# Performance work log

Measured on AMD Instinct MI355X. Metric: run time of the kernel, lower is better.

Reference implementation:

```python
import jax, jax.numpy as jnp
import numpy as np

N_NODES = 10000
T = 8
F_IN = 4
H1 = 16
HEADS = 4
H2 = 32
G = 32
PW = 16
E = 160000


def _gat(x, src, dst, W, a_src, a_dst, b, concat):
    # x: [T, N, Fin]; PyG GATConv (eval mode, dropout inactive), self-loops already in src/dst
    t, n, _ = x.shape
    heads, c = a_src.shape
    z = (x @ W).reshape(t, n, heads, c)                      # [T,N,H,C]
    asrc = jnp.einsum('tnhc,hc->tnh', z, a_src)
    adst = jnp.einsum('tnhc,hc->tnh', z, a_dst)
    e = jax.nn.leaky_relu(asrc[:, src] + adst[:, dst], 0.2)   # [T,E,H]
    e = e.transpose(1, 0, 2)                                  # [E,T,H]
    m = jax.ops.segment_max(e, dst, num_segments=n)           # [N,T,H]
    ex = jnp.exp(e - m[dst])
    s = jax.ops.segment_sum(ex, dst, num_segments=n)
    att = ex / s[dst]                                         # [E,T,H] softmax over in-edges of dst
    msg = z.transpose(1, 0, 2, 3)[src] * att[..., None]       # [E,T,H,C]
    out = jax.ops.segment_sum(msg, dst, num_segments=n)       # [N,T,H,C]
    out = out.transpose(1, 0, 2, 3)                           # [T,N,H,C]
    out = out.reshape(t, n, heads * c) if concat else out.mean(axis=2)
    return out + b


def _forward(dynamic, cI, cR, N, I, R, edge_index, h0,
             W1, att_src1, att_dst1, b1, W2, att_src2, att_dst2, b2,
             W_ih, W_hh, b_ih, b_hh, Wi, bi, Wr, br, Ws, bs):
    Npop = N.squeeze()
    loops = jnp.arange(N_NODES, dtype=edge_index.dtype)
    src = jnp.concatenate([edge_index[0], loops])
    dst = jnp.concatenate([edge_index[1], loops])
    x = dynamic.transpose(1, 0, 2)                            # [T,N,F] all timesteps batched
    x = jax.nn.elu(_gat(x, src, dst, W1, att_src1, att_dst1, b1, True))
    x = jax.nn.elu(_gat(x, src, dst, W2, att_src2, att_dst2, b2, False))
    cur_h = x.mean(axis=1)                                    # [T,H2]

    def gru_step(h, xt):  # torch GRUCell: gates in (r,z,n) order
        gi = W_ih @ xt + b_ih
        gh = W_hh @ h + b_hh
        ir, iz, inn = jnp.split(gi, 3)
        hr, hz, hn = jnp.split(gh, 3)
        r = jax.nn.sigmoid(ir + hr)
        zg = jax.nn.sigmoid(iz + hz)
        ng = jnp.tanh(inn + r * hn)
        hnew = (1.0 - zg) * ng + zg * h
        return hnew, hnew

    h_final, hs = jax.lax.scan(gru_step, h0[0], cur_h)        # hs: [T,G]
    hc = jnp.concatenate([hs, cI[:, None], cR[:, None]], axis=1)  # [T,G+2]
    new_I = (hc @ Wi.T + bi)[None]                            # [1,T,PW]
    new_R = (hc @ Wr.T + br)[None]
    sir = hc @ Ws.T + bs                                      # [T,2]
    alpha = jax.nn.sigmoid(sir[:, 0])
    beta = jax.nn.sigmoid(sir[:, 1])

    def sir_step(carry, _):
        lI, lR = carry
        lS = Npop - lI - lR
        dI = alpha * lI * (lS / Npop) - beta * lI
        dR = beta * lI
        # original accumulates detached increments
        return (lI + jax.lax.stop_gradient(dI), lR + jax.lax.stop_gradient(dR)), (dI, dR)

    _, (dIs, dRs) = jax.lax.scan(sir_step, (I, R), None, length=PW)  # [PW,T]
    phy_I = dIs.T[None]                                       # [1,T,PW]
    phy_R = dRs.T[None]
    return new_I, new_R, phy_I, phy_R, h_final[None]


def setup_inputs() -> dict:
    key = jax.random.key(0)
    ks = jax.random.split(key, 20)
    rn = lambda k, s, sc=0.1: (jax.random.normal(k, s) * sc).astype(jnp.float32)
    return {
        'dynamic': jax.random.normal(ks[0], (N_NODES, T, F_IN), jnp.float32),
        'cI': jax.random.uniform(ks[1], (T,), jnp.float32),
        'cR': jax.random.uniform(ks[2], (T,), jnp.float32),
        'N': jnp.ones((1,), jnp.float32) * 1e6,
        'I': jax.random.uniform(ks[3], (T,), jnp.float32) * 1e4,
        'R': jax.random.uniform(ks[4], (T,), jnp.float32) * 1e4,
        'edge_index': jax.random.randint(ks[5], (2, E), 0, N_NODES, dtype=jnp.int32),
        'h0': rn(ks[6], (1, G)),
        'W1': rn(ks[7], (F_IN, HEADS * H1)),
        'att_src1': rn(ks[8], (HEADS, H1)),
        'att_dst1': rn(ks[9], (HEADS, H1)),
        'b1': jnp.zeros((HEADS * H1,), jnp.float32),
        'W2': rn(ks[10], (HEADS * H1, H2)),
        'att_src2': rn(ks[11], (1, H2)),
        'att_dst2': rn(ks[12], (1, H2)),
        'b2': jnp.zeros((H2,), jnp.float32),
        'W_ih': rn(ks[13], (3 * G, H2)),
        'W_hh': rn(ks[14], (3 * G, G)),
        'b_ih': jnp.zeros((3 * G,), jnp.float32),
        'b_hh': jnp.zeros((3 * G,), jnp.float32),
        'Wi': rn(ks[15], (PW, G + 2)),
        'bi': jnp.zeros((PW,), jnp.float32),
        'Wr': rn(ks[16], (PW, G + 2)),
        'br': jnp.zeros((PW,), jnp.float32),
        'Ws': rn(ks[17], (2, G + 2)),
        'bs': jnp.zeros((2,), jnp.float32),
    }


def reference(dynamic, cI, cR, N, I, R, edge_index, h0,
              W1, att_src1, att_dst1, b1, W2, att_src2, att_dst2, b2,
              W_ih, W_hh, b_ih, b_hh, Wi, bi, Wr, br, Ws, bs):
    return _forward(dynamic, cI, cR, N, I, R, edge_index, h0,
                    W1, att_src1, att_dst1, b1, W2, att_src2, att_dst2, b2,
                    W_ih, W_hh, b_ih, b_hh, Wi, bi, Wr, br, Ws, bs)
```

## Files before the change

kernel.cpp:

```cpp
#include <hip/hip_runtime.h>

#define N_NODES 10000
#define T_STEPS 8
#define F_IN 4
#define H1 16
#define HEADS 4
#define H2 32
#define G 32
#define PW 16
#define E_EDGES 160000
#define ETOT (E_EDGES + N_NODES)
#define NREP 128
#define NGROUP (N_NODES / 4)
#define PZ 0xAAAAAAAAu

__device__ __forceinline__ float lrelu(float x) { return x > 0.f ? x : 0.2f * x; }
__device__ __forceinline__ float eluf(float x) { return x > 0.f ? x : (expf(x) - 1.f); }
__device__ __forceinline__ float sigmoidf(float x) { return 1.f / (1.f + expf(-x)); }
__device__ __forceinline__ float g8max(float v) {
    v = fmaxf(v, __shfl_xor(v, 8));
    v = fmaxf(v, __shfl_xor(v, 16));
    v = fmaxf(v, __shfl_xor(v, 32));
    return v;
}
__device__ __forceinline__ float g8sum(float v) {
    v += __shfl_xor(v, 8);
    v += __shfl_xor(v, 16);
    v += __shfl_xor(v, 32);
    return v;
}
__device__ __forceinline__ float bf2f(unsigned int u) { return __uint_as_float(u << 16); }
__device__ __forceinline__ unsigned short f2bf(float f) {
    unsigned b = __float_as_uint(f);
    return (unsigned short)((b + 0x7FFFu + ((b >> 16) & 1u)) >> 16);
}

__global__ void __launch_bounds__(256) k_count_att(
        const int* __restrict__ ei, unsigned* __restrict__ cnt,
        const float4* __restrict__ dyn, const float* __restrict__ W1,
        const float* __restrict__ as1, const float* __restrict__ ad1,
        float4* __restrict__ asrc, float4* __restrict__ adst,
        float* __restrict__ part, int gEdge, int gTot) {
    for (int i = (int)blockIdx.x * 256 + threadIdx.x; i < NREP * 256; i += gTot * 256)
        part[i] = 0.f;
    if ((int)blockIdx.x < gEdge) {
        int idx = blockIdx.x * 256 + threadIdx.x;
        if (idx >= ETOT) return;
        int dst = (idx < E_EDGES) ? ei[E_EDGES + idx] : (idx - E_EDGES);
        atomicAdd(&cnt[dst], 1u);
    } else {
        __shared__ float VA[16], VD[16];
        int tid = threadIdx.x;
        if (tid < 32) {
            int q = tid & 15, d = q >> 2, h = q & 3;
            const float* a = (tid < 16) ? as1 : ad1;
            float acc = 0.f;
#pragma unroll
            for (int c = 0; c < 16; ++c) acc += W1[d * 64 + h * 16 + c] * a[h * 16 + c];
            if (tid < 16) VA[q] = acc;
            else VD[q] = acc;
        }
        __syncthreads();
        int idx = ((int)blockIdx.x - gEdge) * 256 + tid;
        if (idx >= T_STEPS * N_NODES) return;
        const float4 x = dyn[idx];
        float4 s4, d4;
#pragma unroll
        for (int h = 0; h < 4; ++h) {
            ((float*)&s4)[h] = x.x * VA[h] + x.y * VA[4 + h] + x.z * VA[8 + h] + x.w * VA[12 + h];
            ((float*)&d4)[h] = x.x * VD[h] + x.y * VD[4 + h] + x.z * VD[8 + h] + x.w * VD[12 + h];
        }
        asrc[idx] = s4;
        adst[idx] = d4;
    }
}

__global__ void __launch_bounds__(1024) k_scan(const unsigned* __restrict__ cnt,
                                               int* __restrict__ rowptr,
                                               int* __restrict__ cursor) {
    __shared__ int ssum[1024];
    const int CH = 10;
    int tid = threadIdx.x;
    int base = tid * CH;
    int v[CH];
    int loc = 0;
#pragma unroll
    for (int i = 0; i < CH; ++i) {
        int idx = base + i;
        v[i] = (idx < N_NODES) ? (int)(cnt[idx] - PZ) : 0;
        loc += v[i];
    }
    ssum[tid] = loc;
    __syncthreads();
    for (int st = 1; st < 1024; st <<= 1) {
        int val = (tid >= st) ? ssum[tid - st] : 0;
        __syncthreads();
        ssum[tid] += val;
        __syncthreads();
    }
    int run = ssum[tid] - loc;
#pragma unroll
    for (int i = 0; i < CH; ++i) {
        int idx = base + i;
        if (idx < N_NODES) {
            rowptr[idx] = run;
            cursor[idx] = run;
            run += v[i];
        }
    }
    if (tid == 1023) rowptr[N_NODES] = ssum[1023];
}

__global__ void k_scatter(const int* __restrict__ ei, int* __restrict__ cursor,
                          int* __restrict__ colsrc) {
    int idx = blockIdx.x * blockDim.x + threadIdx.x;
    if (idx >= ETOT) return;
    int src = (idx < E_EDGES) ? ei[idx] : (idx - E_EDGES);
    int dst = (idx < E_EDGES) ? ei[E_EDGES + idx] : (idx - E_EDGES);
    int pos = atomicAdd(&cursor[dst], 1);
    colsrc[pos] = src;
}

__global__ void __launch_bounds__(256) k_l1_node(
        const int* __restrict__ rowptr, const int* __restrict__ colsrc,
        const float4* __restrict__ asrc, const float4* __restrict__ adst,
        const float4* __restrict__ dyn, const float* __restrict__ W1,
        const float* __restrict__ b1, const float* __restrict__ W2,
        const float* __restrict__ as2, const float* __restrict__ ad2,
        unsigned short* __restrict__ z2g, float* __restrict__ asrc2,
        float* __restrict__ adst2) {
    __shared__ float sW1[256], sB1[64], sW2[64 * 32];
    __shared__ float sAs2[32], sAd2[32];
    __shared__ float sRow[4][8 * 65];
    int tid = threadIdx.x;
    for (int i = tid; i < 64 * 32; i += 256) sW2[i] = W2[i];
    sW1[tid] = W1[tid];
    if (tid < 64) sB1[tid] = b1[tid];
    if (tid < 32) { sAs2[tid] = as2[tid]; sAd2[tid] = ad2[tid]; }
    __syncthreads();

    int lane = tid & 63, wslot = tid >> 6;
    int n = blockIdx.x * 4 + wslot;
    int t = lane & 7, es = lane >> 3;
    int beg = rowptr[n];
    int deg = rowptr[n + 1] - beg;
    const float4 ad = adst[(n << 3) + t];

    float m0 = -1e30f, m1 = -1e30f, m2 = -1e30f, m3 = -1e30f;
    float s0 = 0.f, s1 = 0.f, s2 = 0.f, s3 = 0.f;
    float u[16];
#pragma unroll
    for (int i = 0; i < 16; ++i) u[i] = 0.f;

    for (int cb = 0; cb < deg; cb += 24) {
        int cn = deg - cb;
        if (cn > 24) cn = 24;
        int R = (cn + 7) >> 3;
        float4 lr[3], xr[3];
#pragma unroll
        for (int r = 0; r < 3; ++r) {
            lr[r] = make_float4(-1e30f, -1e30f, -1e30f, -1e30f);
            xr[r] = make_float4(0.f, 0.f, 0.f, 0.f);
        }
#pragma unroll
        for (int r = 0; r < 3; ++r) {
            if (r < R) {
                int e = cb + r * 8 + es;
                bool act = e < deg;
                int src = colsrc[beg + (act ? e : 0)];
                const float4 as = asrc[(src << 3) + t];
                const float4 x4 = dyn[(src << 3) + t];
                if (act) {
                    lr[r].x = lrelu(as.x + ad.x);
                    lr[r].y = lrelu(as.y + ad.y);
                    lr[r].z = lrelu(as.z + ad.z);
                    lr[r].w = lrelu(as.w + ad.w);
                    xr[r] = x4;
                }
            }
        }
        float c0 = fmaxf(fmaxf(lr[0].x, lr[1].x), lr[2].x);
        float c1 = fmaxf(fmaxf(lr[0].y, lr[1].y), lr[2].y);
        float c2 = fmaxf(fmaxf(lr[0].z, lr[1].z), lr[2].z);
        float c3 = fmaxf(fmaxf(lr[0].w, lr[1].w), lr[2].w);
        c0 = g8max(c0); c1 = g8max(c1); c2 = g8max(c2); c3 = g8max(c3);
        float nm0 = fmaxf(m0, c0), nm1 = fmaxf(m1, c1);
        float nm2 = fmaxf(m2, c2), nm3 = fmaxf(m3, c3);
        float f0 = expf(m0 - nm0), f1 = expf(m1 - nm1);
        float f2 = expf(m2 - nm2), f3 = expf(m3 - nm3);
        m0 = nm0; m1 = nm1; m2 = nm2; m3 = nm3;
#pragma unroll
        for (int i = 0; i < 16; ++i) u[i] *= (i < 4) ? f0 : (i < 8) ? f1 : (i < 12) ? f2 : f3;
        float ws0 = 0.f, ws1 = 0.f, ws2 = 0.f, ws3 = 0.f;
#pragma unroll
        for (int r = 0; r < 3; ++r) {
            float w0 = expf(lr[r].x - m0);
            float w1 = expf(lr[r].y - m1);
            float w2 = expf(lr[r].z - m2);
            float w3 = expf(lr[r].w - m3);
            ws0 += w0; ws1 += w1; ws2 += w2; ws3 += w3;
            u[0] += w0 * xr[r].x; u[1] += w0 * xr[r].y; u[2] += w0 * xr[r].z; u[3] += w0 * xr[r].w;
            u[4] += w1 * xr[r].x; u[5] += w1 * xr[r].y; u[6] += w1 * xr[r].z; u[7] += w1 * xr[r].w;
            u[8] += w2 * xr[r].x; u[9] += w2 * xr[r].y; u[10] += w2 * xr[r].z; u[11] += w2 * xr[r].w;
            u[12] += w3 * xr[r].x; u[13] += w3 * xr[r].y; u[14] += w3 * xr[r].z; u[15] += w3 * xr[r].w;
        }
        s0 = s0 * f0 + g8sum(ws0);
        s1 = s1 * f1 + g8sum(ws1);
        s2 = s2 * f2 + g8sum(ws2);
        s3 = s3 * f3 + g8sum(ws3);
    }
#pragma unroll
    for (int i = 0; i < 16; ++i) {
        float v = u[i];
        v += __shfl_xor(v, 8);
        v += __shfl_xor(v, 16);
        v += __shfl_xor(v, 32);
        u[i] = v;
    }
    int h = es >> 1;
    float uh0 = (h == 0) ? u[0] : (h == 1) ? u[4] : (h == 2) ? u[8] : u[12];
    float uh1 = (h == 0) ? u[1] : (h == 1) ? u[5] : (h == 2) ? u[9] : u[13];
    float uh2 = (h == 0) ? u[2] : (h == 1) ? u[6] : (h == 2) ? u[10] : u[14];
    float uh3 = (h == 0) ? u[3] : (h == 1) ? u[7] : (h == 2) ? u[11] : u[15];
    float sh = (h == 0) ? s0 : (h == 1) ? s1 : (h == 2) ? s2 : s3;
    float inv = 1.f / sh;
#pragma unroll
    for (int j = 0; j < 8; ++j) {
        int c = es * 8 + j;
        float acc = uh0 * sW1[c] + uh1 * sW1[64 + c] + uh2 * sW1[128 + c] + uh3 * sW1[192 + c];
        sRow[wslot][t * 65 + c] = eluf(acc * inv + sB1[c]);
    }
    __syncthreads();
    float z0 = 0.f, z1v = 0.f, z2v = 0.f, z3v = 0.f;
#pragma unroll 8
    for (int j = 0; j < 64; ++j) {
        float r = sRow[wslot][t * 65 + j];
        const float4 w4 = *reinterpret_cast<const float4*>(&sW2[j * 32 + es * 4]);
        z0 += r * w4.x; z1v += r * w4.y; z2v += r * w4.z; z3v += r * w4.w;
    }
    int wid8 = (n << 3) + t;
    unsigned int p0 = (unsigned)f2bf(z0) | ((unsigned)f2bf(z1v) << 16);
    unsigned int p1 = (unsigned)f2bf(z2v) | ((unsigned)f2bf(z3v) << 16);
    *reinterpret_cast<uint2*>(z2g + (size_t)wid8 * 32 + es * 4) = make_uint2(p0, p1);
    float pa = z0 * sAs2[es * 4] + z1v * sAs2[es * 4 + 1] + z2v * sAs2[es * 4 + 2] + z3v * sAs2[es * 4 + 3];
    float pd = z0 * sAd2[es * 4] + z1v * sAd2[es * 4 + 1] + z2v * sAd2[es * 4 + 2] + z3v * sAd2[es * 4 + 3];
    pa = g8sum(pa);
    pd = g8sum(pd);
    if (es == 0) { asrc2[wid8] = pa; adst2[wid8] = pd; }
}

__global__ void __launch_bounds__(256) k_l2_node(
        const int* __restrict__ rowptr, const int* __restrict__ colsrc,
        const float* __restrict__ asrc, const float* __restrict__ adst,
        const unsigned short* __restrict__ z2, const float* __restrict__ b2,
        float* __restrict__ part) {
    __shared__ int sSrc[4][64];
    __shared__ float sW[4][64 * 8];
    __shared__ float sF[4][8], sS[4][8];
    __shared__ float sB2[32];
    __shared__ float sPart[256];
    int tid = threadIdx.x;
    if (tid < 32) sB2[tid] = b2[tid];
    sPart[tid] = 0.f;
    __syncthreads();

    int lane = tid & 63, wslot = tid >> 6;
    int n = blockIdx.x * 4 + wslot;
    int t = lane & 7, es = lane >> 3;
    int t2 = lane >> 3, cg = lane & 7;
    int beg = rowptr[n];
    int deg = rowptr[n + 1] - beg;
    float ad = adst[(n << 3) + t];
    const unsigned short* zb = z2 + t2 * 32 + cg * 4;

    float m = -1e30f, s = 0.f;
    float a0 = 0.f, a1 = 0.f, a2 = 0.f, a3 = 0.f;
    for (int cb = 0; cb < deg; cb += 64) {
        int cn = deg - cb;
        if (cn > 64) cn = 64;
        int R = (cn + 7) >> 3;
        float lr[8];
#pragma unroll
        for (int r = 0; r < 8; ++r) {
            lr[r] = -1e30f;
            if (r < R) {
                int e = cb + r * 8 + es;
                bool act = e < deg;
                int src = colsrc[beg + (act ? e : 0)];
                if (act) lr[r] = lrelu(asrc[(src << 3) + t] + ad);
                if (t == 0) sSrc[wslot][r * 8 + es] = src;
            }
        }
        float lm = lr[0];
#pragma unroll
        for (int r = 1; r < 8; ++r) lm = fmaxf(lm, lr[r]);
        lm = g8max(lm);
        float nm = fmaxf(m, lm);
        float f = expf(m - nm);
        m = nm;
        float ws = 0.f;
#pragma unroll
        for (int r = 0; r < 8; ++r) {
            if (r < R) {
                float w = expf(lr[r] - nm);
                ws += w;
                sW[wslot][(r * 8 + es) * 8 + t] = w;
            }
        }
        s = s * f + g8sum(ws);
        if (es == 0) sF[wslot][t] = f;
        float fb = sF[wslot][t2];
        a0 *= fb; a1 *= fb; a2 *= fb; a3 *= fb;
        for (int e = 0; e < cn; ++e) {
            int src = sSrc[wslot][e];
            float w = sW[wslot][e * 8 + t2];
            uint2 pz = *reinterpret_cast<const uint2*>(zb + (size_t)src * 256);
            a0 += w * bf2f(pz.x & 0xFFFFu);
            a1 += w * bf2f(pz.x >> 16);
            a2 += w * bf2f(pz.y & 0xFFFFu);
            a3 += w * bf2f(pz.y >> 16);
        }
    }
    if (es == 0) sS[wslot][t] = s;
    float invs = 1.f / sS[wslot][t2];
    int cbase = cg * 4;
    float v0 = eluf(a0 * invs + sB2[cbase]);
    float v1 = eluf(a1 * invs + sB2[cbase + 1]);
    float v2 = eluf(a2 * invs + sB2[cbase + 2]);
    float v3 = eluf(a3 * invs + sB2[cbase + 3]);
    int pidx = t2 * 32 + cbase;
    atomicAdd(&sPart[pidx], v0);
    atomicAdd(&sPart[pidx + 1], v1);
    atomicAdd(&sPart[pidx + 2], v2);
    atomicAdd(&sPart[pidx + 3], v3);
    __syncthreads();
    atomicAdd(&part[((blockIdx.x & (NREP - 1)) << 8) + tid], sPart[tid]);
}

__global__ void k_head(const float* __restrict__ part, const float* __restrict__ h0,
                       const float* __restrict__ W_ih, const float* __restrict__ W_hh,
                       const float* __restrict__ b_ih, const float* __restrict__ b_hh,
                       const float* __restrict__ Wi, const float* __restrict__ bi,
                       const float* __restrict__ Wr, const float* __restrict__ br,
                       const float* __restrict__ Ws, const float* __restrict__ bs,
                       const float* __restrict__ cI, const float* __restrict__ cR,
                       const float* __restrict__ Nptr, const float* __restrict__ Ivec,
                       const float* __restrict__ Rvec, float* __restrict__ out) {
    __shared__ float xs[256];
    __shared__ float h[32], gi[96], gh[96], hnew[32], hs[T_STEPS * 32], sirv[16];
    const float invN = 1.0f / (float)N_NODES;
    int j = threadIdx.x;
#pragma unroll
    for (int p = 0; p < 2; ++p) {
        int e = j + p * 128;
        float sum = 0.f;
        for (int r = 0; r < NREP; ++r) sum += part[r * 256 + e];
        xs[e] = sum * invN;
    }
    if (j < 32) h[j] = h0[j];
    __syncthreads();
    for (int t = 0; t < T_STEPS; ++t) {
        if (j < 96) {
            float accI = b_ih[j], accH = b_hh[j];
            for (int k = 0; k < 32; ++k) {
                accI += W_ih[j * 32 + k] * xs[t * 32 + k];
                accH += W_hh[j * 32 + k] * h[k];
            }
            gi[j] = accI;
            gh[j] = accH;
        }
        __syncthreads();
        if (j < 32) {
            float r = sigmoidf(gi[j] + gh[j]);
            float zg = sigmoidf(gi[32 + j] + gh[32 + j]);
            float ng = tanhf(gi[64 + j] + r * gh[64 + j]);
            hnew[j] = (1.f - zg) * ng + zg * h[j];
        }
        __syncthreads();
        if (j < 32) {
            h[j] = hnew[j];
            hs[t * 32 + j] = hnew[j];
        }
        __syncthreads();
    }
    if (j < 32) out[512 + j] = h[j];
    {
        int t = j >> 4, p = j & 15;
        float accI = bi[p], accR = br[p];
        for (int k = 0; k < 34; ++k) {
            float hck = (k < 32) ? hs[t * 32 + k] : (k == 32 ? cI[t] : cR[t]);
            accI += hck * Wi[p * 34 + k];
            accR += hck * Wr[p * 34 + k];
        }
        out[j] = accI;
        out[128 + j] = accR;
    }
    if (j < 16) {
        int t = j >> 1, q = j & 1;
        float acc = bs[q];
        for (int k = 0; k < 34; ++k) {
            float hck = (k < 32) ? hs[t * 32 + k] : (k == 32 ? cI[t] : cR[t]);
            acc += hck * Ws[q * 34 + k];
        }
        sirv[j] = acc;
    }
    __syncthreads();
    if (j < 8) {
        int t = j;
        float alpha = sigmoidf(sirv[2 * t]);
        float beta = sigmoidf(sirv[2 * t + 1]);
        float Np = Nptr[0];
        float lI = Ivec[t], lR = Rvec[t];
        for (int p = 0; p < PW; ++p) {
            float lS = Np - lI - lR;
            float dI = alpha * lI * (lS / Np) - beta * lI;
            float dR = beta * lI;
            out[256 + t * 16 + p] = dI;
            out[384 + t * 16 + p] = dR;
            lI += dI;
            lR += dR;
        }
    }
}

extern "C" void kernel_launch(void* const* d_in, const int* in_sizes, int n_in,
                              void* d_out, int out_size, void* d_ws, size_t ws_size,
                              hipStream_t stream) {
    const float* dyn = (const float*)d_in[0];
    const float* cI = (const float*)d_in[1];
    const float* cR = (const float*)d_in[2];
    const float* Nptr = (const float*)d_in[3];
    const float* Ivec = (const float*)d_in[4];
    const float* Rvec = (const float*)d_in[5];
    const int* ei = (const int*)d_in[6];
    const float* h0 = (const float*)d_in[7];
    const float* W1 = (const float*)d_in[8];
    const float* as1 = (const float*)d_in[9];
    const float* ad1 = (const float*)d_in[10];
    const float* b1 = (const float*)d_in[11];
    const float* W2 = (const float*)d_in[12];
    const float* as2 = (const float*)d_in[13];
    const float* ad2 = (const float*)d_in[14];
    const float* b2 = (const float*)d_in[15];
    const float* W_ih = (const float*)d_in[16];
    const float* W_hh = (const float*)d_in[17];
    const float* b_ih = (const float*)d_in[18];
    const float* b_hh = (const float*)d_in[19];
    const float* Wi = (const float*)d_in[20];
    const float* bi = (const float*)d_in[21];
    const float* Wr = (const float*)d_in[22];
    const float* br = (const float*)d_in[23];
    const float* Ws = (const float*)d_in[24];
    const float* bs = (const float*)d_in[25];
    float* out = (float*)d_out;

    char* ws = (char*)d_ws;
    size_t off = 0;
    auto alloc = [&](size_t bytes) {
        void* q = ws + off;
        off += (bytes + 255) & ~(size_t)255;
        return q;
    };
    const size_t TN = (size_t)T_STEPS * N_NODES;
    unsigned* cnt = (unsigned*)alloc((N_NODES + 1) * 4);
    float* part = (float*)alloc((size_t)NREP * 256 * 4);
    float4* asrc1 = (float4*)alloc(TN * 16);
    float4* adst1 = (float4*)alloc(TN * 16);
    unsigned short* z2 = (unsigned short*)alloc(TN * 32 * 2);
    float* asrc2 = (float*)alloc(TN * 4);
    float* adst2 = (float*)alloc(TN * 4);
    int* rowptr = (int*)alloc((N_NODES + 1) * 4);
    int* cursor = (int*)alloc(N_NODES * 4);
    int* colsrc = (int*)alloc((size_t)ETOT * 4);
    (void)ws_size; (void)in_sizes; (void)n_in; (void)out_size;

    const int BT = 256;
    int gEdge = (ETOT + BT - 1) / BT;
    int gNode = (int)((TN + BT - 1) / BT);
    k_count_att<<<gEdge + gNode, BT, 0, stream>>>(ei, cnt, (const float4*)dyn, W1, as1, ad1,
                                                  asrc1, adst1, part, gEdge, gEdge + gNode);
    k_scan<<<1, 1024, 0, stream>>>(cnt, rowptr, cursor);
    k_scatter<<<gEdge, BT, 0, stream>>>(ei, cursor, colsrc);
    k_l1_node<<<NGROUP, BT, 0, stream>>>(rowptr, colsrc, asrc1, adst1,
                                         (const float4*)dyn, W1, b1, W2, as2, ad2,
                                         z2, asrc2, adst2);
    k_l2_node<<<NGROUP, BT, 0, stream>>>(rowptr, colsrc, asrc2, adst2, z2, b2, part);
    k_head<<<1, 128, 0, stream>>>(part, h0, W_ih, W_hh, b_ih, b_hh, Wi, bi, Wr, br, Ws, bs,
                                  cI, cR, Nptr, Ivec, Rvec, out);
}
```

Baseline: 214.1 us.

## Fold CSR scan and GRU head into preceding kernels via last-block pattern

The separate single-block scan kernel is folded into the count/attention prep kernel, and the single-block head kernel into the layer-2 node kernel. In each case the last block to finish, found with a global done-counter atomic, does the follow-up work. This removes two kernel launches and their launch gaps from the serial chain. In exchange, the scan now runs on 256 threads with 40 elements each instead of 1024 threads. It also depends on the done counters starting from the poisoned workspace value, with no explicit memory fences before the counter atomics.

```diff
diff --git a/kernel.cpp b/kernel.cpp
--- a/kernel.cpp
+++ b/kernel.cpp
@@ -35,22 +35,29 @@
     return (unsigned short)((b + 0x7FFFu + ((b >> 16) & 1u)) >> 16);
 }
 
-__global__ void __launch_bounds__(256) k_count_att(
+__global__ void __launch_bounds__(256) k_prep(
         const int* __restrict__ ei, unsigned* __restrict__ cnt,
         const float4* __restrict__ dyn, const float* __restrict__ W1,
         const float* __restrict__ as1, const float* __restrict__ ad1,
         float4* __restrict__ asrc, float4* __restrict__ adst,
-        float* __restrict__ part, int gEdge, int gTot) {
-    for (int i = (int)blockIdx.x * 256 + threadIdx.x; i < NREP * 256; i += gTot * 256)
-        part[i] = 0.f;
-    if ((int)blockIdx.x < gEdge) {
-        int idx = blockIdx.x * 256 + threadIdx.x;
-        if (idx >= ETOT) return;
-        int dst = (idx < E_EDGES) ? ei[E_EDGES + idx] : (idx - E_EDGES);
-        atomicAdd(&cnt[dst], 1u);
+        float* __restrict__ part, unsigned* __restrict__ done1,
+        int* __restrict__ rowptr, int* __restrict__ cursor,
+        int gEdge, int gTot) {
+    __shared__ float VA[16], VD[16];
+    __shared__ int ssum[256];
+    __shared__ int isLast;
+    const int tid = threadIdx.x;
+    const int bid = (int)blockIdx.x;
+
+    for (int i = bid * 256 + tid; i < NREP * 256; i += gTot * 256) part[i] = 0.f;
+
+    if (bid < gEdge) {
+        int idx = bid * 256 + tid;
+        if (idx < ETOT) {
+            int dst = (idx < E_EDGES) ? ei[E_EDGES + idx] : (idx - E_EDGES);
+            atomicAdd(&cnt[dst], 1u);
+        }
     } else {
-        __shared__ float VA[16], VD[16];
-        int tid = threadIdx.x;
         if (tid < 32) {
             int q = tid & 15, d = q >> 2, h = q & 3;
             const float* a = (tid < 16) ? as1 : ad1;
@@ -61,54 +68,48 @@
             else VD[q] = acc;
         }
         __syncthreads();
-        int idx = ((int)blockIdx.x - gEdge) * 256 + tid;
-        if (idx >= T_STEPS * N_NODES) return;
-        const float4 x = dyn[idx];
-        float4 s4, d4;
-#pragma unroll
-        for (int h = 0; h < 4; ++h) {
-            ((float*)&s4)[h] = x.x * VA[h] + x.y * VA[4 + h] + x.z * VA[8 + h] + x.w * VA[12 + h];
-            ((float*)&d4)[h] = x.x * VD[h] + x.y * VD[4 + h] + x.z * VD[8 + h] + x.w * VD[12 + h];
-        }
-        asrc[idx] = s4;
-        adst[idx] = d4;
-    }
-}
-
-__global__ void __launch_bounds__(1024) k_scan(const unsigned* __restrict__ cnt,
-                                               int* __restrict__ rowptr,
-                                               int* __restrict__ cursor) {
-    __shared__ int ssum[1024];
-    const int CH = 10;
-    int tid = threadIdx.x;
+        int idx = (bid - gEdge) * 256 + tid;
+        if (idx < T_STEPS * N_NODES) {
+            const float4 x = dyn[idx];
+            float4 s4, d4;
+#pragma unroll
+            for (int h = 0; h < 4; ++h) {
+                ((float*)&s4)[h] = x.x * VA[h] + x.y * VA[4 + h] + x.z * VA[8 + h] + x.w * VA[12 + h];
+                ((float*)&d4)[h] = x.x * VD[h] + x.y * VD[4 + h] + x.z * VD[8 + h] + x.w * VD[12 + h];
+            }
+            asrc[idx] = s4;
+            adst[idx] = d4;
+        }
+    }
+    __syncthreads();
+    if (tid == 0) isLast = (atomicAdd(done1, 1u) == PZ + (unsigned)gTot - 1u);
+    __syncthreads();
+    if (!isLast) return;
+    const int CH = 40;
     int base = tid * CH;
-    int v[CH];
     int loc = 0;
-#pragma unroll
     for (int i = 0; i < CH; ++i) {
         int idx = base + i;
-        v[i] = (idx < N_NODES) ? (int)(cnt[idx] - PZ) : 0;
-        loc += v[i];
+        if (idx < N_NODES) loc += (int)(cnt[idx] - PZ);
     }
     ssum[tid] = loc;
     __syncthreads();
-    for (int st = 1; st < 1024; st <<= 1) {
-        int val = (tid >= st) ? ssum[tid - st] : 0;
-        __syncthreads();
-        ssum[tid] += val;
+    for (int st = 1; st < 256; st <<= 1) {
+        int v = (tid >= st) ? ssum[tid - st] : 0;
+        __syncthreads();
+        ssum[tid] += v;
         __syncthreads();
     }
     int run = ssum[tid] - loc;
-#pragma unroll
     for (int i = 0; i < CH; ++i) {
         int idx = base + i;
         if (idx < N_NODES) {
             rowptr[idx] = run;
             cursor[idx] = run;
-            run += v[i];
-        }
-    }
-    if (tid == 1023) rowptr[N_NODES] = ssum[1023];
+            run += (int)(cnt[idx] - PZ);
+        }
+    }
+    if (tid == 255) rowptr[N_NODES] = ssum[255];
 }
 
 __global__ void k_scatter(const int* __restrict__ ei, int* __restrict__ cursor,
@@ -249,19 +250,32 @@
     if (es == 0) { asrc2[wid8] = pa; adst2[wid8] = pd; }
 }
 
+struct SL2b {
+    int sSrc[4][64];
+    float sW[4][64 * 8], sF[4][8], sS[4][8], sB2[32], sPart[256];
+};
+struct SHd {
+    float xs[256], h[32], gi[96], gh[96], hnew[32], hs[256], sirv[16];
+};
 __global__ void __launch_bounds__(256) k_l2_node(
         const int* __restrict__ rowptr, const int* __restrict__ colsrc,
         const float* __restrict__ asrc, const float* __restrict__ adst,
         const unsigned short* __restrict__ z2, const float* __restrict__ b2,
-        float* __restrict__ part) {
-    __shared__ int sSrc[4][64];
-    __shared__ float sW[4][64 * 8];
-    __shared__ float sF[4][8], sS[4][8];
-    __shared__ float sB2[32];
-    __shared__ float sPart[256];
+        float* __restrict__ part, unsigned* __restrict__ done2,
+        const float* __restrict__ h0,
+        const float* __restrict__ W_ih, const float* __restrict__ W_hh,
+        const float* __restrict__ b_ih, const float* __restrict__ b_hh,
+        const float* __restrict__ Wi, const float* __restrict__ bi,
+        const float* __restrict__ Wr, const float* __restrict__ br,
+        const float* __restrict__ Ws, const float* __restrict__ bs,
+        const float* __restrict__ cI, const float* __restrict__ cR,
+        const float* __restrict__ Nptr, const float* __restrict__ Iv,
+        const float* __restrict__ Rv, float* __restrict__ out) {
+    __shared__ union { SL2b l2; SHd hd; } su;
+    __shared__ int isLast;
     int tid = threadIdx.x;
-    if (tid < 32) sB2[tid] = b2[tid];
-    sPart[tid] = 0.f;
+    if (tid < 32) su.l2.sB2[tid] = b2[tid];
+    su.l2.sPart[tid] = 0.f;
     __syncthreads();
 
     int lane = tid & 63, wslot = tid >> 6;
@@ -288,7 +302,7 @@
                 bool act = e < deg;
                 int src = colsrc[beg + (act ? e : 0)];
                 if (act) lr[r] = lrelu(asrc[(src << 3) + t] + ad);
-                if (t == 0) sSrc[wslot][r * 8 + es] = src;
+                if (t == 0) su.l2.sSrc[wslot][r * 8 + es] = src;
             }
         }
         float lm = lr[0];
@@ -298,22 +312,22 @@
         float nm = fmaxf(m, lm);
         float f = expf(m - nm);
         m = nm;
-        float ws = 0.f;
+        float wsm = 0.f;
 #pragma unroll
         for (int r = 0; r < 8; ++r) {
             if (r < R) {
                 float w = expf(lr[r] - nm);
-                ws += w;
-                sW[wslot][(r * 8 + es) * 8 + t] = w;
+                wsm += w;
+                su.l2.sW[wslot][(r * 8 + es) * 8 + t] = w;
             }
         }
-        s = s * f + g8sum(ws);
-        if (es == 0) sF[wslot][t] = f;
-        float fb = sF[wslot][t2];
+        s = s * f + g8sum(wsm);
+        if (es == 0) su.l2.sF[wslot][t] = f;
+        float fb = su.l2.sF[wslot][t2];
         a0 *= fb; a1 *= fb; a2 *= fb; a3 *= fb;
         for (int e = 0; e < cn; ++e) {
-            int src = sSrc[wslot][e];
-            float w = sW[wslot][e * 8 + t2];
+            int src = su.l2.sSrc[wslot][e];
+            float w = su.l2.sW[wslot][e * 8 + t2];
             uint2 pz = *reinterpret_cast<const uint2*>(zb + (size_t)src * 256);
             a0 += w * bf2f(pz.x & 0xFFFFu);
             a1 += w * bf2f(pz.x >> 16);
@@ -321,102 +335,92 @@
             a3 += w * bf2f(pz.y >> 16);
         }
     }
-    if (es == 0) sS[wslot][t] = s;
-    float invs = 1.f / sS[wslot][t2];
+    if (es == 0) su.l2.sS[wslot][t] = s;
+    float invs = 1.f / su.l2.sS[wslot][t2];
     int cbase = cg * 4;
-    float v0 = eluf(a0 * invs + sB2[cbase]);
-    float v1 = eluf(a1 * invs + sB2[cbase + 1]);
-    float v2 = eluf(a2 * invs + sB2[cbase + 2]);
-    float v3 = eluf(a3 * invs + sB2[cbase + 3]);
+    float v0 = eluf(a0 * invs + su.l2.sB2[cbase]);
+    float v1 = eluf(a1 * invs + su.l2.sB2[cbase + 1]);
+    float v2 = eluf(a2 * invs + su.l2.sB2[cbase + 2]);
+    float v3 = eluf(a3 * invs + su.l2.sB2[cbase + 3]);
     int pidx = t2 * 32 + cbase;
-    atomicAdd(&sPart[pidx], v0);
-    atomicAdd(&sPart[pidx + 1], v1);
-    atomicAdd(&sPart[pidx + 2], v2);
-    atomicAdd(&sPart[pidx + 3], v3);
-    __syncthreads();
-    atomicAdd(&part[((blockIdx.x & (NREP - 1)) << 8) + tid], sPart[tid]);
-}
-
-__global__ void k_head(const float* __restrict__ part, const float* __restrict__ h0,
-                       const float* __restrict__ W_ih, const float* __restrict__ W_hh,
-                       const float* __restrict__ b_ih, const float* __restrict__ b_hh,
-                       const float* __restrict__ Wi, const float* __restrict__ bi,
-                       const float* __restrict__ Wr, const float* __restrict__ br,
-                       const float* __restrict__ Ws, const float* __restrict__ bs,
-                       const float* __restrict__ cI, const float* __restrict__ cR,
-                       const float* __restrict__ Nptr, const float* __restrict__ Ivec,
-                       const float* __restrict__ Rvec, float* __restrict__ out) {
-    __shared__ float xs[256];
-    __shared__ float h[32], gi[96], gh[96], hnew[32], hs[T_STEPS * 32], sirv[16];
+    atomicAdd(&su.l2.sPart[pidx], v0);
+    atomicAdd(&su.l2.sPart[pidx + 1], v1);
+    atomicAdd(&su.l2.sPart[pidx + 2], v2);
+    atomicAdd(&su.l2.sPart[pidx + 3], v3);
+    __syncthreads();
+    float myPart = su.l2.sPart[tid];
+    atomicAdd(&part[(((int)blockIdx.x & (NREP - 1)) << 8) + tid], myPart);
+
+    __syncthreads();
+    if (tid == 0) isLast = (atomicAdd(done2, 1u) == PZ + NGROUP - 1u);
+    __syncthreads();
+    if (!isLast) return;
     const float invN = 1.0f / (float)N_NODES;
-    int j = threadIdx.x;
-#pragma unroll
-    for (int p = 0; p < 2; ++p) {
-        int e = j + p * 128;
+    {
         float sum = 0.f;
-        for (int r = 0; r < NREP; ++r) sum += part[r * 256 + e];
-        xs[e] = sum * invN;
-    }
-    if (j < 32) h[j] = h0[j];
-    __syncthreads();
-    for (int t = 0; t < T_STEPS; ++t) {
-        if (j < 96) {
-            float accI = b_ih[j], accH = b_hh[j];
+        for (int r = 0; r < NREP; ++r) sum += part[r * 256 + tid];
+        su.hd.xs[tid] = sum * invN;
+    }
+    if (tid < 32) su.hd.h[tid] = h0[tid];
+    __syncthreads();
+    for (int tt = 0; tt < T_STEPS; ++tt) {
+        if (tid < 96) {
+            float accI = b_ih[tid], accH = b_hh[tid];
             for (int k = 0; k < 32; ++k) {
-                accI += W_ih[j * 32 + k] * xs[t * 32 + k];
-                accH += W_hh[j * 32 + k] * h[k];
+                accI += W_ih[tid * 32 + k] * su.hd.xs[tt * 32 + k];
+                accH += W_hh[tid * 32 + k] * su.hd.h[k];
             }
-            gi[j] = accI;
-            gh[j] = accH;
-        }
-        __syncthreads();
-        if (j < 32) {
-            float r = sigmoidf(gi[j] + gh[j]);
-            float zg = sigmoidf(gi[32 + j] + gh[32 + j]);
-            float ng = tanhf(gi[64 + j] + r * gh[64 + j]);
-            hnew[j] = (1.f - zg) * ng + zg * h[j];
-        }
-        __syncthreads();
-        if (j < 32) {
-            h[j] = hnew[j];
-            hs[t * 32 + j] = hnew[j];
-        }
-        __syncthreads();
-    }
-    if (j < 32) out[512 + j] = h[j];
-    {
-        int t = j >> 4, p = j & 15;
-        float accI = bi[p], accR = br[p];
+            su.hd.gi[tid] = accI;
+            su.hd.gh[tid] = accH;
+        }
+        __syncthreads();
+        if (tid < 32) {
+            float r = sigmoidf(su.hd.gi[tid] + su.hd.gh[tid]);
+            float zg = sigmoidf(su.hd.gi[32 + tid] + su.hd.gh[32 + tid]);
+            float ng = tanhf(su.hd.gi[64 + tid] + r * su.hd.gh[64 + tid]);
+            su.hd.hnew[tid] = (1.f - zg) * ng + zg * su.hd.h[tid];
+        }
+        __syncthreads();
+        if (tid < 32) {
+            su.hd.h[tid] = su.hd.hnew[tid];
+            su.hd.hs[tt * 32 + tid] = su.hd.hnew[tid];
+        }
+        __syncthreads();
+    }
+    if (tid < 32) out[512 + tid] = su.hd.h[tid];
+    if (tid < 128) {
+        int tt = tid >> 4, q = tid & 15;
+        float accI = bi[q], accR = br[q];
         for (int k = 0; k < 34; ++k) {
-            float hck = (k < 32) ? hs[t * 32 + k] : (k == 32 ? cI[t] : cR[t]);
-            accI += hck * Wi[p * 34 + k];
-            accR += hck * Wr[p * 34 + k];
-        }
-        out[j] = accI;
-        out[128 + j] = accR;
-    }
-    if (j < 16) {
-        int t = j >> 1, q = j & 1;
+            float hck = (k < 32) ? su.hd.hs[tt * 32 + k] : (k == 32 ? cI[tt] : cR[tt]);
+            accI += hck * Wi[q * 34 + k];
+            accR += hck * Wr[q * 34 + k];
+        }
+        out[tid] = accI;
+        out[128 + tid] = accR;
+    }
+    if (tid < 16) {
+        int tt = tid >> 1, q = tid & 1;
         float acc = bs[q];
         for (int k = 0; k < 34; ++k) {
-            float hck = (k < 32) ? hs[t * 32 + k] : (k == 32 ? cI[t] : cR[t]);
+            float hck = (k < 32) ? su.hd.hs[tt * 32 + k] : (k == 32 ? cI[tt] : cR[tt]);
             acc += hck * Ws[q * 34 + k];
         }
-        sirv[j] = acc;
-    }
-    __syncthreads();
-    if (j < 8) {
-        int t = j;
-        float alpha = sigmoidf(sirv[2 * t]);
-        float beta = sigmoidf(sirv[2 * t + 1]);
+        su.hd.sirv[tid] = acc;
+    }
+    __syncthreads();
+    if (tid < 8) {
+        int tt = tid;
+        float alpha = sigmoidf(su.hd.sirv[2 * tt]);
+        float beta = sigmoidf(su.hd.sirv[2 * tt + 1]);
         float Np = Nptr[0];
-        float lI = Ivec[t], lR = Rvec[t];
-        for (int p = 0; p < PW; ++p) {
+        float lI = Iv[tt], lR = Rv[tt];
+        for (int q = 0; q < PW; ++q) {
             float lS = Np - lI - lR;
             float dI = alpha * lI * (lS / Np) - beta * lI;
             float dR = beta * lI;
-            out[256 + t * 16 + p] = dI;
-            out[384 + t * 16 + p] = dR;
+            out[256 + tt * 16 + q] = dI;
+            out[384 + tt * 16 + q] = dR;
             lI += dI;
             lR += dR;
         }
@@ -464,6 +468,8 @@
     const size_t TN = (size_t)T_STEPS * N_NODES;
     unsigned* cnt = (unsigned*)alloc((N_NODES + 1) * 4);
     float* part = (float*)alloc((size_t)NREP * 256 * 4);
+    unsigned* done1 = (unsigned*)alloc(256);
+    unsigned* done2 = (unsigned*)(((char*)done1) + 128);
     float4* asrc1 = (float4*)alloc(TN * 16);
     float4* adst1 = (float4*)alloc(TN * 16);
     unsigned short* z2 = (unsigned short*)alloc(TN * 32 * 2);
@@ -477,14 +483,14 @@
     const int BT = 256;
     int gEdge = (ETOT + BT - 1) / BT;
     int gNode = (int)((TN + BT - 1) / BT);
-    k_count_att<<<gEdge + gNode, BT, 0, stream>>>(ei, cnt, (const float4*)dyn, W1, as1, ad1,
-                                                  asrc1, adst1, part, gEdge, gEdge + gNode);
-    k_scan<<<1, 1024, 0, stream>>>(cnt, rowptr, cursor);
+    k_prep<<<gEdge + gNode, BT, 0, stream>>>(ei, cnt, (const float4*)dyn, W1, as1, ad1,
+                                             asrc1, adst1, part, done1, rowptr, cursor,
+                                             gEdge, gEdge + gNode);
     k_scatter<<<gEdge, BT, 0, stream>>>(ei, cursor, colsrc);
     k_l1_node<<<NGROUP, BT, 0, stream>>>(rowptr, colsrc, asrc1, adst1,
                                          (const float4*)dyn, W1, b1, W2, as2, ad2,
                                          z2, asrc2, adst2);
-    k_l2_node<<<NGROUP, BT, 0, stream>>>(rowptr, colsrc, asrc2, adst2, z2, b2, part);
-    k_head<<<1, 128, 0, stream>>>(part, h0, W_ih, W_hh, b_ih, b_hh, Wi, bi, Wr, br, Ws, bs,
-                                  cI, cR, Nptr, Ivec, Rvec, out);
-}
+    k_l2_node<<<NGROUP, BT, 0, stream>>>(rowptr, colsrc, asrc2, adst2, z2, b2, part, done2,
+                                         h0, W_ih, W_hh, b_ih, b_hh, Wi, bi, Wr, br, Ws, bs,
+                                         cI, cR, Nptr, Ivec, Rvec, out);
+}
```

Result: slower. 248.8 us (+16.2%).
